# Kernel optimization log

Hardware: AMD Instinct MI355X
Metric: run time of the kernel (lower is better)

## Reference

```python
import jax, jax.numpy as jnp
import numpy as np

OBJ_DIM, REL_DIM, EFF_DIM = 5, 1, 100
REL_HID, OBJ_HID, OUT_DIM = 150, 100, 2


def _init_linear(key, fan_in, fan_out):
    kw, kb = jax.random.split(key)
    bound = 1.0 / np.sqrt(fan_in)
    W = jax.random.uniform(kw, (fan_in, fan_out), jnp.float32, -bound, bound)
    b = jax.random.uniform(kb, (fan_out,), jnp.float32, -bound, bound)
    return W, b


def setup_inputs() -> dict:
    key = jax.random.key(0)
    ks = jax.random.split(key, 12)
    B, N, R = 64, 100, 9900
    inp = {
        "objects": jax.random.normal(ks[0], (B, N, OBJ_DIM), jnp.float32),
        "sender_relations": jax.random.uniform(ks[1], (B, N, R), jnp.float32),
        "receiver_relations": jax.random.uniform(ks[2], (B, N, R), jnp.float32),
        "relation_info": jax.random.normal(ks[3], (B, R, REL_DIM), jnp.float32),
    }
    # relational MLP: (2*obj + rel) -> 150 -> 150 -> effect_dim, ReLU after each
    rW1, rb1 = _init_linear(ks[4], 2 * OBJ_DIM + REL_DIM, REL_HID)
    rW2, rb2 = _init_linear(ks[5], REL_HID, REL_HID)
    rW3, rb3 = _init_linear(ks[6], REL_HID, EFF_DIM)
    # object MLP: (obj + effect) -> 100 -> 100 -> 2
    oW1, ob1 = _init_linear(ks[7], OBJ_DIM + EFF_DIM, OBJ_HID)
    oW2, ob2 = _init_linear(ks[8], OBJ_HID, OBJ_HID)
    oW3, ob3 = _init_linear(ks[9], OBJ_HID, OUT_DIM)
    inp.update(rW1=rW1, rb1=rb1, rW2=rW2, rb2=rb2, rW3=rW3, rb3=rb3,
               oW1=oW1, ob1=ob1, oW2=oW2, ob2=ob2, oW3=oW3, ob3=ob3)
    return inp


def _relational_mlp(x, rW1, rb1, rW2, rb2, rW3, rb3):
    h = jax.nn.relu(x @ rW1 + rb1)
    h = jax.nn.relu(h @ rW2 + rb2)
    return jax.nn.relu(h @ rW3 + rb3)


def _object_mlp(x, oW1, ob1, oW2, ob2, oW3, ob3):
    h = jax.nn.relu(x @ oW1 + ob1)
    h = jax.nn.relu(h @ oW2 + ob2)
    return h @ oW3 + ob3


def reference(objects, sender_relations, receiver_relations, relation_info,
              rW1, rb1, rW2, rb2, rW3, rb3, oW1, ob1, oW2, ob2, oW3, ob3):
    # gather: [B,R,N] @ [B,N,D] -> [B,R,D]
    senders = jnp.einsum('bnr,bnd->brd', sender_relations, objects)
    receivers = jnp.einsum('bnr,bnd->brd', receiver_relations, objects)
    rel_in = jnp.concatenate([senders, receivers, relation_info], axis=2)
    effects = _relational_mlp(rel_in, rW1, rb1, rW2, rb2, rW3, rb3)  # [B,R,E]
    # scatter: [B,N,R] @ [B,R,E] -> [B,N,E]
    effect_receivers = jnp.einsum('bnr,bre->bne', receiver_relations, effects)
    obj_in = jnp.concatenate([objects, effect_receivers], axis=2)
    return _object_mlp(obj_in, oW1, ob1, oW2, ob2, oW3, ob3)  # [B,N,2]
```

## Files before the change

kernel.cpp:

```cpp
#include <hip/hip_runtime.h>
#include <hip/hip_bf16.h>

#define B_    64
#define N_    100
#define R_    9900
#define OBJD  5
#define EFF   100

typedef __bf16 bf16x8 __attribute__((ext_vector_type(8)));
typedef __bf16 bf16x2 __attribute__((ext_vector_type(2)));
typedef float  f32x4  __attribute__((ext_vector_type(4)));

__device__ __forceinline__ ushort f2bf(float f) {
    __bf16 h = (__bf16)f;
    return __builtin_bit_cast(ushort, h);
}
__device__ __forceinline__ unsigned pk2(float a, float b) {
    bf16x2 v; v[0] = (__bf16)a; v[1] = (__bf16)b;
    return __builtin_bit_cast(unsigned, v);
}
__device__ __forceinline__ float bf2f(ushort u) {
    union { unsigned u; float f; } x; x.u = ((unsigned)u) << 16;
    return x.f;
}

#define WTR_OBJ 52096
#define W2F_OFF 144256
#define W3F_OFF 169856

__global__ __launch_bounds__(256) void k_prepw(
    const float* __restrict__ W1, const float* __restrict__ W2,
    const float* __restrict__ W3, const float* __restrict__ O1,
    const float* __restrict__ O2, const float* __restrict__ O3,
    ushort* __restrict__ WTR)
{
    const int img = blockIdx.x;
    if (img == 0) {
        for (int idx = threadIdx.x; idx < 6400; idx += 256) {
            const int c = idx / 40, k = idx - (idx/40)*40;
            WTR[idx] = f2bf((c < 150 && k < 11) ? W1[k*150 + c] : 0.f);
        }
    } else if (img == 1) {
        for (int idx = threadIdx.x; idx < 26880; idx += 256) {
            const int c = idx / 168, k = idx - (idx/168)*168;
            WTR[6400 + idx] = f2bf((c < 150 && k < 150) ? W2[k*150 + c] : 0.f);
        }
    } else if (img == 2) {
        for (int idx = threadIdx.x; idx < 18816; idx += 256) {
            const int c = idx / 168, k = idx - (idx/168)*168;
            WTR[33280 + idx] = f2bf((c < 100 && k < 150) ? W3[k*100 + c] : 0.f);
        }
    } else if (img == 11) {
        for (int idx = threadIdx.x; idx < 25600; idx += 256) {
            const int ctks = idx >> 9;
            const int ct = ctks / 5, ks = ctks - ct*5;
            const int lane = (idx >> 3) & 63, e = idx & 7;
            const int c = ct*16 + (lane & 15);
            const int k = ks*32 + (lane >> 4)*8 + e;
            WTR[W2F_OFF + idx] = f2bf((c < 150 && k < 150) ? W2[k*150 + c] : 0.f);
        }
    } else if (img == 12) {
        for (int idx = threadIdx.x; idx < 17920; idx += 256) {
            const int ctks = idx >> 9;
            const int ct = ctks / 5, ks = ctks - ct*5;
            const int lane = (idx >> 3) & 63, e = idx & 7;
            const int c = ct*16 + (lane & 15);
            const int k = ks*32 + (lane >> 4)*8 + e;
            WTR[W3F_OFF + idx] = f2bf((c < 100 && k < 150) ? W3[k*100 + c] : 0.f);
        }
    } else {
        const int j = img - 3;
        ushort* dst = WTR + WTR_OBJ + (size_t)j*11520;
        for (int idx = threadIdx.x; idx < 11520; idx += 256) {
            const int cc = idx / 72, kk = idx - (idx/72)*72;
            float v = 0.f;
            if (kk < 64) {
                if (j < 4) {
                    const int kg = j*64 + kk;
                    int row = -1;
                    if (kg < 5) row = kg;
                    else if (kg >= 8 && kg < 108) row = kg - 3;
                    else if (kg >= 108 && kg < 208) row = kg - 103;
                    if (cc < 100 && row >= 0) v = O1[row*100 + cc];
                } else if (j < 6) {
                    const int kg = (j-4)*64 + kk;
                    if (cc < 100 && kg < 100) v = O2[kg*100 + cc];
                } else {
                    const int kg = (j-6)*64 + kk;
                    if (cc < 2 && kg < 100) v = O3[kg*2 + cc];
                }
            }
            dst[idx] = f2bf(v);
        }
    }
}

#define LW1   0
#define LBA   6400
#define LBB   14464
#define LACT  22528
#define LBIAS 33280
#define LGB   34080
#define LTOT  35616

__global__ __launch_bounds__(512, 2) void k_relmlp_p(
    const float* __restrict__ obj, const float* __restrict__ SR,
    const float* __restrict__ RR, const float* __restrict__ RI,
    const ushort* __restrict__ WTR,
    const float* __restrict__ b1, const float* __restrict__ b2,
    const float* __restrict__ b3, float* __restrict__ ER)
{
    __shared__ __align__(16) ushort lds[LTOT];
    const int t   = threadIdx.x;
    const int b   = blockIdx.x >> 3;
    const int oct = blockIdx.x & 7;
    const int lane = t & 63, w = t >> 6;
    const int lo = lane & 15, hi = lane >> 4;
    const int mt = w & 3, nh = w >> 2;
    const int q  = t & 7,  rr = t >> 3;

    ushort* bufA = lds + LBA;
    ushort* bufB = lds + LBB;
    ushort* act  = lds + LACT;
    ushort* gb   = lds + LGB;
    const float* bias = (const float*)(lds + LBIAS);

    #pragma unroll
    for (int j = 0; j < 2; ++j) {
        const int idx = t + j*512;
        if (idx < 800)
            reinterpret_cast<uint4*>(lds)[idx] =
                reinterpret_cast<const uint4*>(WTR)[idx];
    }
    {
        float* bias_w = (float*)(lds + LBIAS);
        if (t < 150)      bias_w[t] = b1[t];
        else if (t < 300) bias_w[t] = b2[t-150];
        else if (t < 400) bias_w[t] = b3[t-300];
    }
    if (t < 216) {
        ushort* base = ((t < 108) ? bufA : bufB) + 100*72;
        const int k = (t < 108) ? t : t - 108;
        *reinterpret_cast<uint4*>(base + k*8) = make_uint4(0u, 0u, 0u, 0u);
    }
    if (t < 64) {
        ushort* gb0 = gb + t*24;
        gb0[11] = 0;
        *reinterpret_cast<ushort4*>(&gb0[12]) = make_ushort4(0,0,0,0);
        *reinterpret_cast<ushort4*>(&gb0[16]) = make_ushort4(0,0,0,0);
        *reinterpret_cast<ushort4*>(&gb0[20]) = make_ushort4(0,0,0,0);
    }

    float objv[13][5];
    {
        const int n0 = q*13;
        #pragma unroll
        for (int i = 0; i < 13; ++i) {
            const int n = n0 + i;
            #pragma unroll
            for (int d = 0; d < 5; ++d)
                objv[i][d] = (n < N_) ? obj[(size_t)b*500 + n*5 + d] : 0.f;
        }
    }

    const int tile0 = (oct*155) >> 3;
    const int tile1 = ((oct+1)*155) >> 3;

    f32x4 acc_er[7];
    #pragma unroll
    for (int ct = 0; ct < 7; ++ct) acc_er[ct] = (f32x4){0.f, 0.f, 0.f, 0.f};

    float4 psr[4], prr[4];
    float pri = 0.f, pri_n = 0.f;
    auto load4 = [&](float4* p, const float* M, int tile) {
        const int rr0 = tile*64;
        const int nr = (R_ - rr0 < 64) ? R_ - rr0 : 64;
        #pragma unroll
        for (int i = 0; i < 4; ++i) {
            const int idx = t + i*512;
            const int ci = idx < 1600 ? idx : 1599;
            const int n = ci >> 4, qq = ci & 15;
            const int col = (qq*4 < nr) ? qq*4 : 0;
            p[i] = *reinterpret_cast<const float4*>(
                &M[((size_t)b*N_ + n)*R_ + rr0 + col]);
        }
    };
    auto store4 = [&](const float4* p, ushort* dst, int nrow) {
        #pragma unroll
        for (int i = 0; i < 4; ++i) {
            const int idx = t + i*512;
            if (idx < 1600) {
                const int n = idx >> 4, qq = idx & 15;
                float4 v = p[i];
                if (qq*4 >= nrow) v = make_float4(0.f, 0.f, 0.f, 0.f);
                uint2 u; u.x = pk2(v.x, v.y); u.y = pk2(v.z, v.w);
                *reinterpret_cast<uint2*>(&dst[n*72 + qq*4]) = u;
            }
        }
    };
    auto loadRI = [&](int tile) -> float {
        const int rr0 = tile*64;
        return (t < 64 && rr0 + t < R_) ? RI[(size_t)b*R_ + rr0 + t] : 0.f;
    };

    load4(psr, SR, tile0);
    load4(prr, RR, tile0);
    pri = loadRI(tile0);
    __syncthreads();

    for (int tile = tile0; tile < tile1; ++tile) {
        const int r0 = tile*64;
        const int nrow = (R_ - r0 < 64) ? R_ - r0 : 64;

        store4(psr, bufA, nrow);
        store4(prr, bufB, nrow);
        if (tile + 1 < tile1) {
            load4(psr, SR, tile+1);
            load4(prr, RR, tile+1);
            pri_n = loadRI(tile+1);
        }
        __syncthreads();

        {
            float s0=0.f,s1=0.f,s2=0.f,s3=0.f,s4=0.f;
            float g0=0.f,g1=0.f,g2=0.f,g3=0.f,g4=0.f;
            const int n0 = q*13;
            #pragma unroll
            for (int i = 0; i < 13; ++i) {
                const int n = n0 + i;
                const float ms = bf2f(bufA[n*72 + rr]);
                const float mr = bf2f(bufB[n*72 + rr]);
                s0 += ms*objv[i][0]; s1 += ms*objv[i][1]; s2 += ms*objv[i][2];
                s3 += ms*objv[i][3]; s4 += ms*objv[i][4];
                g0 += mr*objv[i][0]; g1 += mr*objv[i][1]; g2 += mr*objv[i][2];
                g3 += mr*objv[i][3]; g4 += mr*objv[i][4];
            }
            #pragma unroll
            for (int msk = 1; msk < 8; msk <<= 1) {
                s0 += __shfl_xor(s0, msk); s1 += __shfl_xor(s1, msk);
                s2 += __shfl_xor(s2, msk); s3 += __shfl_xor(s3, msk);
                s4 += __shfl_xor(s4, msk);
                g0 += __shfl_xor(g0, msk); g1 += __shfl_xor(g1, msk);
                g2 += __shfl_xor(g2, msk); g3 += __shfl_xor(g3, msk);
                g4 += __shfl_xor(g4, msk);
            }
            if (q < 5) {
                const float sv = (q==0)?s0:(q==1)?s1:(q==2)?s2:(q==3)?s3:s4;
                const float gv = (q==0)?g0:(q==1)?g1:(q==2)?g2:(q==3)?g3:g4;
                gb[rr*24 + q]     = f2bf(sv);
                gb[rr*24 + 5 + q] = f2bf(gv);
            }
            if (t < 64) gb[t*24 + 10] = f2bf(pri);
            pri = pri_n;
        }
        __syncthreads();

        {
            f32x4 acc[5];
            #pragma unroll
            for (int j = 0; j < 5; ++j) {
                const int c = (nh*5 + j)*16 + lo;
                const float bv = (c < 150) ? bias[c] : 0.f;
                acc[j][0]=bv; acc[j][1]=bv; acc[j][2]=bv; acc[j][3]=bv;
            }
            bf16x8 a = {};
            if (hi < 2)
                a = *reinterpret_cast<const bf16x8*>(
                    &gb[(mt*16 + lo)*24 + hi*8]);
            #pragma unroll
            for (int j = 0; j < 5; ++j) {
                const int ct = nh*5 + j;
                const bf16x8 bb = *reinterpret_cast<const bf16x8*>(
                    &lds[LW1 + (ct*16 + lo)*40 + hi*8]);
                acc[j] = __builtin_amdgcn_mfma_f32_16x16x32_bf16(a, bb, acc[j], 0,0,0);
            }
            #pragma unroll
            for (int j = 0; j < 5; ++j) {
                const int ct = nh*5 + j;
                #pragma unroll
                for (int r = 0; r < 4; ++r)
                    act[(mt*16 + hi*4 + r)*168 + ct*16 + lo] =
                        f2bf(fmaxf(acc[j][r], 0.f));
            }
            __syncthreads();
        }
        {
            const ushort* w2p = WTR + W2F_OFF + (size_t)lane*8 + (size_t)nh*12800;
            asm volatile("" : "+v"(w2p));
            f32x4 acc[5];
            #pragma unroll
            for (int j = 0; j < 5; ++j) {
                const int c = (nh*5 + j)*16 + lo;
                const float bv = (c < 150) ? bias[150 + c] : 0.f;
                acc[j][0]=bv; acc[j][1]=bv; acc[j][2]=bv; acc[j][3]=bv;
            }
            #pragma unroll
            for (int ks = 0; ks < 5; ++ks) {
                const bf16x8 a = *reinterpret_cast<const bf16x8*>(
                    &act[(mt*16 + lo)*168 + ks*32 + hi*8]);
                const bf16x8 b0  = *reinterpret_cast<const bf16x8*>(w2p + ((0*5 + ks) << 9));
                const bf16x8 b1v = *reinterpret_cast<const bf16x8*>(w2p + ((1*5 + ks) << 9));
                const bf16x8 b2v = *reinterpret_cast<const bf16x8*>(w2p + ((2*5 + ks) << 9));
                const bf16x8 b3v = *reinterpret_cast<const bf16x8*>(w2p + ((3*5 + ks) << 9));
                const bf16x8 b4v = *reinterpret_cast<const bf16x8*>(w2p + ((4*5 + ks) << 9));
                acc[0] = __builtin_amdgcn_mfma_f32_16x16x32_bf16(a, b0,  acc[0], 0,0,0);
                acc[1] = __builtin_amdgcn_mfma_f32_16x16x32_bf16(a, b1v, acc[1], 0,0,0);
                acc[2] = __builtin_amdgcn_mfma_f32_16x16x32_bf16(a, b2v, acc[2], 0,0,0);
                acc[3] = __builtin_amdgcn_mfma_f32_16x16x32_bf16(a, b3v, acc[3], 0,0,0);
                acc[4] = __builtin_amdgcn_mfma_f32_16x16x32_bf16(a, b4v, acc[4], 0,0,0);
            }
            __syncthreads();
            #pragma unroll
            for (int j = 0; j < 5; ++j) {
                const int ct = nh*5 + j;
                #pragma unroll
                for (int r = 0; r < 4; ++r)
                    act[(mt*16 + hi*4 + r)*168 + ct*16 + lo] =
                        f2bf(fmaxf(acc[j][r], 0.f));
            }
            __syncthreads();
        }
        {
            const ushort* w3p = WTR + W3F_OFF + (size_t)lane*8 + (size_t)nh*10240;
            asm volatile("" : "+v"(w3p));
            const int nct = nh ? 3 : 4;
            f32x4 acc[4];
            #pragma unroll
            for (int j = 0; j < 4; ++j) {
                const int c = (nh*4 + j)*16 + lo;
                const float bv = (c < 100) ? bias[300 + c] : 0.f;
                acc[j][0]=bv; acc[j][1]=bv; acc[j][2]=bv; acc[j][3]=bv;
            }
            #pragma unroll
            for (int ks = 0; ks < 5; ++ks) {
                const bf16x8 a = *reinterpret_cast<const bf16x8*>(
                    &act[(mt*16 + lo)*168 + ks*32 + hi*8]);
                #pragma unroll
                for (int j = 0; j < 4; ++j) {
                    if (j < nct) {
                        const bf16x8 bb = *reinterpret_cast<const bf16x8*>(
                            w3p + ((j*5 + ks) << 9));
                        acc[j] = __builtin_amdgcn_mfma_f32_16x16x32_bf16(a, bb, acc[j], 0,0,0);
                    }
                }
            }
            #pragma unroll
            for (int j = 0; j < 4; ++j) {
                if (j < nct) {
                    const int e = (nh*4 + j)*16 + lo;
                    if (e < 100) {
                        uint2 u;
                        u.x = pk2(fmaxf(acc[j][0], 0.f), fmaxf(acc[j][1], 0.f));
                        u.y = pk2(fmaxf(acc[j][2], 0.f), fmaxf(acc[j][3], 0.f));
                        *reinterpret_cast<uint2*>(&bufA[e*72 + mt*16 + hi*4]) = u;
                    }
                }
            }
            __syncthreads();
        }

        if (w < 7) {
            #pragma unroll
            for (int ks = 0; ks < 2; ++ks) {
                const bf16x8 a = *reinterpret_cast<const bf16x8*>(
                    &bufB[(w*16 + lo)*72 + ks*32 + hi*8]);
                #pragma unroll
                for (int ct = 0; ct < 7; ++ct) {
                    const bf16x8 bb = *reinterpret_cast<const bf16x8*>(
                        &bufA[(ct*16 + lo)*72 + ks*32 + hi*8]);
                    acc_er[ct] = __builtin_amdgcn_mfma_f32_16x16x32_bf16(
                        a, bb, acc_er[ct], 0, 0, 0);
                }
            }
        }
        __syncthreads();
    }

    if (w < 7) {
        float* ERq = ER + ((size_t)oct*B_ + b)*(size_t)(N_*EFF);
        #pragma unroll
        for (int ct = 0; ct < 7; ++ct) {
            const int e = ct*16 + lo;
            if (e < EFF) {
                #pragma unroll
                for (int rg = 0; rg < 4; ++rg) {
                    const int n = w*16 + hi*4 + rg;
                    if (n < N_)
                        ERq[n*EFF + e] = acc_er[ct][rg];
                }
            }
        }
    }
}

__device__ __forceinline__ void img_load(const ushort* __restrict__ g,
                                         uint4* pre, int t) {
    #pragma unroll
    for (int j = 0; j < 6; ++j) {
        int idx = t + j*256;
        int cidx = idx < 1440 ? idx : 1439;
        pre[j] = *reinterpret_cast<const uint4*>(g + (size_t)cidx*8);
    }
}
__device__ __forceinline__ void img_store(const uint4* pre, ushort* wt, int t) {
    #pragma unroll
    for (int j = 0; j < 6; ++j) {
        int idx = t + j*256;
        if (idx < 1440)
            *reinterpret_cast<uint4*>(wt + (size_t)idx*8) = pre[j];
    }
}

template<int COUT, int NCHUNK, int LASTKS, int NCT, bool RELU, int EPI, int ASTR>
__device__ __forceinline__ void mfma_layerO(
    const ushort* __restrict__ WT, const float* __restrict__ Bias,
    ushort* act, ushort* wt, int t, float* gout, int grow0)
{
    const int lane = t & 63;
    const int wv   = t >> 6;
    const int lo   = lane & 15;
    const int hi   = lane >> 4;

    f32x4 acc[2][NCT];
    #pragma unroll
    for (int ct = 0; ct < NCT; ++ct) {
        const int c = ct*16 + lo;
        const float bv = (c < COUT) ? Bias[c] : 0.f;
        #pragma unroll
        for (int m = 0; m < 2; ++m) {
            acc[m][ct][0] = bv; acc[m][ct][1] = bv;
            acc[m][ct][2] = bv; acc[m][ct][3] = bv;
        }
    }

    uint4 pre[6];
    img_load(WT, pre, t);
    #pragma unroll
    for (int q = 0; q < NCHUNK; ++q) {
        __syncthreads();
        img_store(pre, wt, t);
        if (q + 1 < NCHUNK) img_load(WT + (size_t)(q+1)*11520, pre, t);
        __syncthreads();
        const int nks = (q == NCHUNK-1) ? LASTKS : 2;
        #pragma unroll
        for (int ks = 0; ks < 2; ++ks) {
            if (ks < nks) {
                const int kg = q*64 + ks*32;
                const bf16x8 a0 = *reinterpret_cast<const bf16x8*>(
                    &act[(wv*32 +      lo)*ASTR + kg + hi*8]);
                const bf16x8 a1 = *reinterpret_cast<const bf16x8*>(
                    &act[(wv*32 + 16 + lo)*ASTR + kg + hi*8]);
                #pragma unroll
                for (int ct = 0; ct < NCT; ++ct) {
                    const bf16x8 b = *reinterpret_cast<const bf16x8*>(
                        &wt[(ct*16 + lo)*72 + ks*32 + hi*8]);
                    acc[0][ct] = __builtin_amdgcn_mfma_f32_16x16x32_bf16(
                        a0, b, acc[0][ct], 0, 0, 0);
                    acc[1][ct] = __builtin_amdgcn_mfma_f32_16x16x32_bf16(
                        a1, b, acc[1][ct], 0, 0, 0);
                }
            }
        }
    }

    __syncthreads();
    if (EPI == 0) {
        #pragma unroll
        for (int m = 0; m < 2; ++m)
            #pragma unroll
            for (int ct = 0; ct < NCT; ++ct)
                #pragma unroll
                for (int r = 0; r < 4; ++r) {
                    float v = acc[m][ct][r];
                    if (RELU) v = fmaxf(v, 0.f);
                    act[(wv*32 + m*16 + hi*4 + r)*ASTR + ct*16 + lo] = f2bf(v);
                }
    } else {
        #pragma unroll
        for (int m = 0; m < 2; ++m)
            #pragma unroll
            for (int r = 0; r < 4; ++r)
                if (lo < 2)
                    gout[(size_t)(grow0 + wv*32 + m*16 + hi*4 + r)*2 + lo] =
                        acc[m][0][r];
    }
    __syncthreads();
}

#define OSTR 232
#define ERSL ((size_t)B_*N_*EFF)

__global__ __launch_bounds__(256, 1) void k_objmlp_mfma(
    const float* __restrict__ obj, const float* __restrict__ ER,
    const ushort* __restrict__ WO,
    const float* __restrict__ ob1, const float* __restrict__ ob2,
    const float* __restrict__ ob3, float* __restrict__ out)
{
    __shared__ __align__(16) ushort act[128*OSTR];
    __shared__ __align__(16) ushort wt[160*72];
    const int t = threadIdx.x;
    const int rowbase = blockIdx.x * 128;

    float4 per[13];
    #pragma unroll
    for (int j = 0; j < 13; ++j) {
        const int idx = t + j*256;
        const int ci = idx < 3200 ? idx : 3199;
        const int row = ci / 25, c = ci - row*25;
        const float* p = &ER[(size_t)(rowbase + row)*100 + c*4];
        float4 s = make_float4(0.f, 0.f, 0.f, 0.f);
        #pragma unroll
        for (int sl = 0; sl < 8; ++sl) {
            const float4 a = *reinterpret_cast<const float4*>(p + (size_t)sl*ERSL);
            s.x += a.x; s.y += a.y; s.z += a.z; s.w += a.w;
        }
        per[j] = s;
    }
    #pragma unroll
    for (int j = 0; j < 13; ++j) {
        const int idx = t + j*256;
        if (idx < 3200) {
            const int row = idx / 25, c = idx - row*25;
            ushort h[4], l[4];
            #pragma unroll
            for (int k = 0; k < 4; ++k) {
                const float f = ((const float*)&per[j])[k];
                h[k] = f2bf(f);
                l[k] = f2bf(f - bf2f(h[k]));
            }
            *reinterpret_cast<ushort4*>(&act[row*OSTR + 8 + c*4]) =
                make_ushort4(h[0], h[1], h[2], h[3]);
            *reinterpret_cast<ushort4*>(&act[row*OSTR + 108 + c*4]) =
                make_ushort4(l[0], l[1], l[2], l[3]);
        }
    }
    #pragma unroll
    for (int j = 0; j < 3; ++j) {
        const int idx = t + j*256;
        if (idx < 640) {
            const int row = idx / 5, d = idx - row*5;
            act[row*OSTR + d] = f2bf(obj[(size_t)(rowbase + row)*5 + d]);
        }
    }
    #pragma unroll
    for (int j = 0; j < 2; ++j) {
        const int idx = t + j*256;
        if (idx < 384) {
            const int row = idx / 3, c = 5 + (idx - row*3);
            act[row*OSTR + c] = 0;
        }
    }
    #pragma unroll
    for (int j = 0; j < 2; ++j) {
        const int idx = t + j*256;
        if (idx < 512) {
            const int row = idx >> 2, p = idx & 3;
            *reinterpret_cast<ushort4*>(&act[row*OSTR + 208 + p*4]) =
                make_ushort4(0, 0, 0, 0);
        }
    }

    mfma_layerO<100, 4, 1, 7, true,  0, OSTR>(WO,           ob1, act, wt, t, nullptr, 0);
    mfma_layerO<100, 2, 2, 7, true,  0, OSTR>(WO + 4*11520, ob2, act, wt, t, nullptr, 0);
    mfma_layerO<2,   2, 2, 1, false, 2, OSTR>(WO + 6*11520, ob3, act, wt, t, out, rowbase);
}

extern "C" void kernel_launch(void* const* d_in, const int* in_sizes, int n_in,
                              void* d_out, int out_size, void* d_ws, size_t ws_size,
                              hipStream_t stream)
{
    const float* objects = (const float*)d_in[0];
    const float* SR      = (const float*)d_in[1];
    const float* RR      = (const float*)d_in[2];
    const float* RI      = (const float*)d_in[3];
    const float* rW1 = (const float*)d_in[4];  const float* rb1 = (const float*)d_in[5];
    const float* rW2 = (const float*)d_in[6];  const float* rb2 = (const float*)d_in[7];
    const float* rW3 = (const float*)d_in[8];  const float* rb3 = (const float*)d_in[9];
    const float* oW1 = (const float*)d_in[10]; const float* ob1 = (const float*)d_in[11];
    const float* oW2 = (const float*)d_in[12]; const float* ob2 = (const float*)d_in[13];
    const float* oW3 = (const float*)d_in[14]; const float* ob3 = (const float*)d_in[15];
    float* out = (float*)d_out;

    char* ws = (char*)d_ws;
    float*  ERp = (float*)ws;
    ushort* WTR = (ushort*)(ws + (size_t)8*B_*N_*EFF*sizeof(float));

    k_prepw<<<dim3(13), 256, 0, stream>>>(rW1, rW2, rW3, oW1, oW2, oW3, WTR);

    k_relmlp_p<<<dim3(512), 512, 0, stream>>>(objects, SR, RR, RI, WTR,
                                              rb1, rb2, rb3, ERp);

    k_objmlp_mfma<<<dim3(50), 256, 0, stream>>>(objects, ERp, WTR + WTR_OBJ,
                                                ob1, ob2, ob3, out);
}
```

Before: 399.5 us.

## Compute sender/receiver gather with MFMA via transposed LDS tiles

Replaces the scalar per-thread gather (objv register array, dot products, shuffle reductions) with MFMA matmuls. SR and RR tiles are stored transposed in LDS and multiplied against bf16 objects held in LDS. W1 fragments are prepacked in MFMA layout and read from global memory instead of LDS. The cost is an extra global load per element of RR (both a transposed copy and the original layout), strided scalar global loads for the transposed tiles, and a larger LDS footprint, all meant to cut VALU and shuffle work.

```diff
diff --git a/kernel.cpp b/kernel.cpp
--- a/kernel.cpp
+++ b/kernel.cpp
@@ -27,6 +27,7 @@
 #define WTR_OBJ 52096
 #define W2F_OFF 144256
 #define W3F_OFF 169856
+#define W1F_OFF 187776
 
 __global__ __launch_bounds__(256) void k_prepw(
     const float* __restrict__ W1, const float* __restrict__ W2,
@@ -67,6 +68,14 @@
             const int c = ct*16 + (lane & 15);
             const int k = ks*32 + (lane >> 4)*8 + e;
             WTR[W3F_OFF + idx] = f2bf((c < 100 && k < 150) ? W3[k*100 + c] : 0.f);
+        }
+    } else if (img == 13) {
+        for (int idx = threadIdx.x; idx < 5120; idx += 256) {
+            const int ct = idx >> 9;
+            const int lane = (idx >> 3) & 63, e = idx & 7;
+            const int c = ct*16 + (lane & 15);
+            const int k = (lane >> 4)*8 + e;
+            WTR[W1F_OFF + idx] = f2bf((c < 150 && k < 11) ? W1[k*150 + c] : 0.f);
         }
     } else {
         const int j = img - 3;
@@ -95,13 +104,15 @@
     }
 }
 
-#define LW1   0
-#define LBA   6400
-#define LBB   14464
-#define LACT  22528
-#define LBIAS 33280
-#define LGB   34080
-#define LTOT  35616
+#define STRT  136
+#define LSRT  0
+#define LRRT  8704
+#define LBB   17408
+#define LACT  25472
+#define LBIAS 36224
+#define LGB   37024
+#define LOBJ  38560
+#define LTOT  40736
 
 __global__ __launch_bounds__(512, 2) void k_relmlp_p(
     const float* __restrict__ obj, const float* __restrict__ SR,
@@ -117,20 +128,29 @@
     const int lane = t & 63, w = t >> 6;
     const int lo = lane & 15, hi = lane >> 4;
     const int mt = w & 3, nh = w >> 2;
-    const int q  = t & 7,  rr = t >> 3;
-
-    ushort* bufA = lds + LBA;
-    ushort* bufB = lds + LBB;
+
+    ushort* SRT  = lds + LSRT;
+    ushort* RRT  = lds + LRRT;
+    ushort* RRn  = lds + LBB;
+    ushort* EB   = lds + LSRT;
     ushort* act  = lds + LACT;
     ushort* gb   = lds + LGB;
+    ushort* lobj = lds + LOBJ;
     const float* bias = (const float*)(lds + LBIAS);
 
     #pragma unroll
-    for (int j = 0; j < 2; ++j) {
+    for (int j = 0; j < 5; ++j) {
         const int idx = t + j*512;
-        if (idx < 800)
-            reinterpret_cast<uint4*>(lds)[idx] =
-                reinterpret_cast<const uint4*>(WTR)[idx];
+        if (idx < 2176)
+            reinterpret_cast<uint4*>(lds)[idx] = make_uint4(0u,0u,0u,0u);
+    }
+    #pragma unroll
+    for (int j = 0; j < 5; ++j) {
+        const int idx = t + j*512;
+        if (idx < 2176) {
+            const int d = idx / STRT, n = idx - d*STRT;
+            lobj[idx] = f2bf((d < 5 && n < N_) ? obj[(size_t)b*500 + n*5 + d] : 0.f);
+        }
     }
     {
         float* bias_w = (float*)(lds + LBIAS);
@@ -138,10 +158,8 @@
         else if (t < 300) bias_w[t] = b2[t-150];
         else if (t < 400) bias_w[t] = b3[t-300];
     }
-    if (t < 216) {
-        ushort* base = ((t < 108) ? bufA : bufB) + 100*72;
-        const int k = (t < 108) ? t : t - 108;
-        *reinterpret_cast<uint4*>(base + k*8) = make_uint4(0u, 0u, 0u, 0u);
+    if (t < 108) {
+        *reinterpret_cast<uint4*>(RRn + 100*72 + t*8) = make_uint4(0u,0u,0u,0u);
     }
     if (t < 64) {
         ushort* gb0 = gb + t*24;
@@ -151,27 +169,33 @@
         *reinterpret_cast<ushort4*>(&gb0[20]) = make_ushort4(0,0,0,0);
     }
 
-    float objv[13][5];
-    {
-        const int n0 = q*13;
+    const int tile0 = (oct*155) >> 3;
+    const int tile1 = ((oct+1)*155) >> 3;
+
+    f32x4 acc_er[7];
+    #pragma unroll
+    for (int ct = 0; ct < 7; ++ct) acc_er[ct] = (f32x4){0.f, 0.f, 0.f, 0.f};
+
+    float vs[13], vr[13];
+    auto loadT = [&](float* v, const float* M, int tile) {
+        const int rr0 = tile*64;
+        const int r = t & 63, g = t >> 6;
+        const int n0 = g*13;
+        const bool rok = (rr0 + r < R_);
         #pragma unroll
         for (int i = 0; i < 13; ++i) {
             const int n = n0 + i;
-            #pragma unroll
-            for (int d = 0; d < 5; ++d)
-                objv[i][d] = (n < N_) ? obj[(size_t)b*500 + n*5 + d] : 0.f;
-        }
-    }
-
-    const int tile0 = (oct*155) >> 3;
-    const int tile1 = ((oct+1)*155) >> 3;
-
-    f32x4 acc_er[7];
-    #pragma unroll
-    for (int ct = 0; ct < 7; ++ct) acc_er[ct] = (f32x4){0.f, 0.f, 0.f, 0.f};
-
-    float4 psr[4], prr[4];
-    float pri = 0.f, pri_n = 0.f;
+            v[i] = (rok && n < N_) ? M[((size_t)b*N_ + n)*R_ + rr0 + r] : 0.f;
+        }
+    };
+    auto storeT = [&](const float* v, ushort* dst) {
+        const int r = t & 63, g = t >> 6;
+        const int n0 = g*13;
+        #pragma unroll
+        for (int i = 0; i < 13; ++i)
+            dst[r*STRT + n0 + i] = f2bf(v[i]);
+    };
+    float4 prr[4];
     auto load4 = [&](float4* p, const float* M, int tile) {
         const int rr0 = tile*64;
         const int nr = (R_ - rr0 < 64) ? R_ - rr0 : 64;
@@ -203,52 +227,43 @@
         return (t < 64 && rr0 + t < R_) ? RI[(size_t)b*R_ + rr0 + t] : 0.f;
     };
 
-    load4(psr, SR, tile0);
+    loadT(vs, SR, tile0);
+    loadT(vr, RR, tile0);
     load4(prr, RR, tile0);
-    pri = loadRI(tile0);
+    float pri = loadRI(tile0), pri_n = 0.f;
     __syncthreads();
 
     for (int tile = tile0; tile < tile1; ++tile) {
         const int r0 = tile*64;
         const int nrow = (R_ - r0 < 64) ? R_ - r0 : 64;
 
-        store4(psr, bufA, nrow);
-        store4(prr, bufB, nrow);
+        storeT(vs, SRT);
+        storeT(vr, RRT);
+        store4(prr, RRn, nrow);
         if (tile + 1 < tile1) {
-            load4(psr, SR, tile+1);
+            loadT(vs, SR, tile+1);
+            loadT(vr, RR, tile+1);
             load4(prr, RR, tile+1);
             pri_n = loadRI(tile+1);
         }
         __syncthreads();
 
         {
-            float s0=0.f,s1=0.f,s2=0.f,s3=0.f,s4=0.f;
-            float g0=0.f,g1=0.f,g2=0.f,g3=0.f,g4=0.f;
-            const int n0 = q*13;
-            #pragma unroll
-            for (int i = 0; i < 13; ++i) {
-                const int n = n0 + i;
-                const float ms = bf2f(bufA[n*72 + rr]);
-                const float mr = bf2f(bufB[n*72 + rr]);
-                s0 += ms*objv[i][0]; s1 += ms*objv[i][1]; s2 += ms*objv[i][2];
-                s3 += ms*objv[i][3]; s4 += ms*objv[i][4];
-                g0 += mr*objv[i][0]; g1 += mr*objv[i][1]; g2 += mr*objv[i][2];
-                g3 += mr*objv[i][3]; g4 += mr*objv[i][4];
-            }
-            #pragma unroll
-            for (int msk = 1; msk < 8; msk <<= 1) {
-                s0 += __shfl_xor(s0, msk); s1 += __shfl_xor(s1, msk);
-                s2 += __shfl_xor(s2, msk); s3 += __shfl_xor(s3, msk);
-                s4 += __shfl_xor(s4, msk);
-                g0 += __shfl_xor(g0, msk); g1 += __shfl_xor(g1, msk);
-                g2 += __shfl_xor(g2, msk); g3 += __shfl_xor(g3, msk);
-                g4 += __shfl_xor(g4, msk);
-            }
-            if (q < 5) {
-                const float sv = (q==0)?s0:(q==1)?s1:(q==2)?s2:(q==3)?s3:s4;
-                const float gv = (q==0)?g0:(q==1)?g1:(q==2)?g2:(q==3)?g3:g4;
-                gb[rr*24 + q]     = f2bf(sv);
-                gb[rr*24 + 5 + q] = f2bf(gv);
+            const int which = w >> 2;
+            const ushort* At = which ? RRT : SRT;
+            f32x4 g = (f32x4){0.f, 0.f, 0.f, 0.f};
+            #pragma unroll
+            for (int ks = 0; ks < 4; ++ks) {
+                const bf16x8 a = *reinterpret_cast<const bf16x8*>(
+                    &At[(mt*16 + lo)*STRT + ks*32 + hi*8]);
+                const bf16x8 bO = *reinterpret_cast<const bf16x8*>(
+                    &lobj[lo*STRT + ks*32 + hi*8]);
+                g = __builtin_amdgcn_mfma_f32_16x16x32_bf16(a, bO, g, 0,0,0);
+            }
+            if (lo < 5) {
+                #pragma unroll
+                for (int r = 0; r < 4; ++r)
+                    gb[(mt*16 + hi*4 + r)*24 + which*5 + lo] = f2bf(g[r]);
             }
             if (t < 64) gb[t*24 + 10] = f2bf(pri);
             pri = pri_n;
@@ -256,6 +271,8 @@
         __syncthreads();
 
         {
+            const ushort* w1p = WTR + W1F_OFF + (size_t)lane*8;
+            asm volatile("" : "+v"(w1p));
             f32x4 acc[5];
             #pragma unroll
             for (int j = 0; j < 5; ++j) {
@@ -270,8 +287,7 @@
             #pragma unroll
             for (int j = 0; j < 5; ++j) {
                 const int ct = nh*5 + j;
-                const bf16x8 bb = *reinterpret_cast<const bf16x8*>(
-                    &lds[LW1 + (ct*16 + lo)*40 + hi*8]);
+                const bf16x8 bb = *reinterpret_cast<const bf16x8*>(w1p + ct*512);
                 acc[j] = __builtin_amdgcn_mfma_f32_16x16x32_bf16(a, bb, acc[j], 0,0,0);
             }
             #pragma unroll
@@ -348,12 +364,12 @@
             for (int j = 0; j < 4; ++j) {
                 if (j < nct) {
                     const int e = (nh*4 + j)*16 + lo;
+                    uint2 u = make_uint2(0u, 0u);
                     if (e < 100) {
-                        uint2 u;
                         u.x = pk2(fmaxf(acc[j][0], 0.f), fmaxf(acc[j][1], 0.f));
                         u.y = pk2(fmaxf(acc[j][2], 0.f), fmaxf(acc[j][3], 0.f));
-                        *reinterpret_cast<uint2*>(&bufA[e*72 + mt*16 + hi*4]) = u;
                     }
+                    *reinterpret_cast<uint2*>(&EB[e*72 + mt*16 + hi*4]) = u;
                 }
             }
             __syncthreads();
@@ -363,11 +379,11 @@
             #pragma unroll
             for (int ks = 0; ks < 2; ++ks) {
                 const bf16x8 a = *reinterpret_cast<const bf16x8*>(
-                    &bufB[(w*16 + lo)*72 + ks*32 + hi*8]);
+                    &RRn[(w*16 + lo)*72 + ks*32 + hi*8]);
                 #pragma unroll
                 for (int ct = 0; ct < 7; ++ct) {
                     const bf16x8 bb = *reinterpret_cast<const bf16x8*>(
-                        &bufA[(ct*16 + lo)*72 + ks*32 + hi*8]);
+                        &EB[(ct*16 + lo)*72 + ks*32 + hi*8]);
                     acc_er[ct] = __builtin_amdgcn_mfma_f32_16x16x32_bf16(
                         a, bb, acc_er[ct], 0, 0, 0);
                 }
@@ -585,7 +601,7 @@
     float*  ERp = (float*)ws;
     ushort* WTR = (ushort*)(ws + (size_t)8*B_*N_*EFF*sizeof(float));
 
-    k_prepw<<<dim3(13), 256, 0, stream>>>(rW1, rW2, rW3, oW1, oW2, oW3, WTR);
+    k_prepw<<<dim3(14), 256, 0, stream>>>(rW1, rW2, rW3, oW1, oW2, oW3, WTR);
 
     k_relmlp_p<<<dim3(512), 512, 0, stream>>>(objects, SR, RR, RI, WTR,
                                               rb1, rb2, rb3, ERp);
```

Result: slower. 429.6 us (+7.5%).

## Warp-specialize relational MLP kernel into compute and load/scatter warp groups

Applied to the files above, without the earlier changes.

Splits the 8 waves of the relational-MLP block into two roles. Waves 0-3 run the gather and the three MLP layers on 16-row slices each, with per-wave activation buffers. Waves 4-7 stage the next tile of sender/receiver matrices into double-buffered LDS and perform the scatter MFMA for the previous tile, leaving one barrier per tile. This is meant to overlap global loads and the scatter with MLP compute and remove several barriers. In exchange LDS use roughly doubles and launch bounds drop to one block per CU, which lowers occupancy.

```diff
diff --git a/kernel.cpp b/kernel.cpp
--- a/kernel.cpp
+++ b/kernel.cpp
@@ -96,14 +96,19 @@
 }
 
 #define LW1   0
-#define LBA   6400
-#define LBB   14464
-#define LACT  22528
-#define LBIAS 33280
-#define LGB   34080
-#define LTOT  35616
-
-__global__ __launch_bounds__(512, 2) void k_relmlp_p(
+#define LSR0  6400
+#define LSR1  14464
+#define LRR0  22528
+#define LRR1  30592
+#define LEB0  38656
+#define LEB1  46720
+#define LACT1 54784
+#define LACT2 65536
+#define LGB   76288
+#define LBIAS 77824
+#define LTOT  78624
+
+__global__ __launch_bounds__(512, 1) void k_relmlp_p(
     const float* __restrict__ obj, const float* __restrict__ SR,
     const float* __restrict__ RR, const float* __restrict__ RI,
     const ushort* __restrict__ WTR,
@@ -116,14 +121,10 @@
     const int oct = blockIdx.x & 7;
     const int lane = t & 63, w = t >> 6;
     const int lo = lane & 15, hi = lane >> 4;
-    const int mt = w & 3, nh = w >> 2;
-    const int q  = t & 7,  rr = t >> 3;
-
-    ushort* bufA = lds + LBA;
-    ushort* bufB = lds + LBB;
-    ushort* act  = lds + LACT;
-    ushort* gb   = lds + LGB;
+
     const float* bias = (const float*)(lds + LBIAS);
+    const int tile0 = (oct*155) >> 3;
+    const int tile1 = ((oct+1)*155) >> 3;
 
     #pragma unroll
     for (int j = 0; j < 2; ++j) {
@@ -138,255 +139,278 @@
         else if (t < 300) bias_w[t] = b2[t-150];
         else if (t < 400) bias_w[t] = b3[t-300];
     }
-    if (t < 216) {
-        ushort* base = ((t < 108) ? bufA : bufB) + 100*72;
-        const int k = (t < 108) ? t : t - 108;
-        *reinterpret_cast<uint4*>(base + k*8) = make_uint4(0u, 0u, 0u, 0u);
+    #pragma unroll
+    for (int j = 0; j < 2; ++j) {
+        const int idx = t + j*512;
+        if (idx < 648) {
+            const int bsel = idx / 108, kk = idx - bsel*108;
+            *reinterpret_cast<uint4*>(lds + LSR0 + bsel*8064 + 100*72 + kk*8) =
+                make_uint4(0u, 0u, 0u, 0u);
+        }
     }
     if (t < 64) {
-        ushort* gb0 = gb + t*24;
+        ushort* gb0 = lds + LGB + (t >> 4)*384 + (t & 15)*24;
         gb0[11] = 0;
         *reinterpret_cast<ushort4*>(&gb0[12]) = make_ushort4(0,0,0,0);
         *reinterpret_cast<ushort4*>(&gb0[16]) = make_ushort4(0,0,0,0);
         *reinterpret_cast<ushort4*>(&gb0[20]) = make_ushort4(0,0,0,0);
     }
 
-    float objv[13][5];
-    {
-        const int n0 = q*13;
-        #pragma unroll
-        for (int i = 0; i < 13; ++i) {
-            const int n = n0 + i;
-            #pragma unroll
-            for (int d = 0; d < 5; ++d)
-                objv[i][d] = (n < N_) ? obj[(size_t)b*500 + n*5 + d] : 0.f;
-        }
-    }
-
-    const int tile0 = (oct*155) >> 3;
-    const int tile1 = ((oct+1)*155) >> 3;
-
-    f32x4 acc_er[7];
-    #pragma unroll
-    for (int ct = 0; ct < 7; ++ct) acc_er[ct] = (f32x4){0.f, 0.f, 0.f, 0.f};
-
-    float4 psr[4], prr[4];
-    float pri = 0.f, pri_n = 0.f;
-    auto load4 = [&](float4* p, const float* M, int tile) {
+    const int tS = t - 256;
+    auto stage = [&](int tile, int pp) {
         const int rr0 = tile*64;
         const int nr = (R_ - rr0 < 64) ? R_ - rr0 : 64;
-        #pragma unroll
-        for (int i = 0; i < 4; ++i) {
-            const int idx = t + i*512;
-            const int ci = idx < 1600 ? idx : 1599;
-            const int n = ci >> 4, qq = ci & 15;
-            const int col = (qq*4 < nr) ? qq*4 : 0;
-            p[i] = *reinterpret_cast<const float4*>(
-                &M[((size_t)b*N_ + n)*R_ + rr0 + col]);
-        }
-    };
-    auto store4 = [&](const float4* p, ushort* dst, int nrow) {
-        #pragma unroll
-        for (int i = 0; i < 4; ++i) {
-            const int idx = t + i*512;
+        ushort* dS = lds + (pp ? LSR1 : LSR0);
+        ushort* dR = lds + (pp ? LRR1 : LRR0);
+        #pragma unroll
+        for (int i = 0; i < 7; ++i) {
+            const int idx = tS + i*256;
             if (idx < 1600) {
                 const int n = idx >> 4, qq = idx & 15;
-                float4 v = p[i];
-                if (qq*4 >= nrow) v = make_float4(0.f, 0.f, 0.f, 0.f);
+                const int col = (qq*4 < nr) ? qq*4 : 0;
+                float4 v = *reinterpret_cast<const float4*>(
+                    &SR[((size_t)b*N_ + n)*R_ + rr0 + col]);
+                if (qq*4 >= nr) v = make_float4(0.f, 0.f, 0.f, 0.f);
                 uint2 u; u.x = pk2(v.x, v.y); u.y = pk2(v.z, v.w);
-                *reinterpret_cast<uint2*>(&dst[n*72 + qq*4]) = u;
+                *reinterpret_cast<uint2*>(&dS[n*72 + qq*4]) = u;
+                float4 v2 = *reinterpret_cast<const float4*>(
+                    &RR[((size_t)b*N_ + n)*R_ + rr0 + col]);
+                if (qq*4 >= nr) v2 = make_float4(0.f, 0.f, 0.f, 0.f);
+                uint2 u2; u2.x = pk2(v2.x, v2.y); u2.y = pk2(v2.z, v2.w);
+                *reinterpret_cast<uint2*>(&dR[n*72 + qq*4]) = u2;
             }
         }
     };
-    auto loadRI = [&](int tile) -> float {
-        const int rr0 = tile*64;
-        return (t < 64 && rr0 + t < R_) ? RI[(size_t)b*R_ + rr0 + t] : 0.f;
-    };
-
-    load4(psr, SR, tile0);
-    load4(prr, RR, tile0);
-    pri = loadRI(tile0);
+
+    if (w >= 4) stage(tile0, tile0 & 1);
     __syncthreads();
 
-    for (int tile = tile0; tile < tile1; ++tile) {
-        const int r0 = tile*64;
-        const int nrow = (R_ - r0 < 64) ? R_ - r0 : 64;
-
-        store4(psr, bufA, nrow);
-        store4(prr, bufB, nrow);
-        if (tile + 1 < tile1) {
-            load4(psr, SR, tile+1);
-            load4(prr, RR, tile+1);
-            pri_n = loadRI(tile+1);
-        }
-        __syncthreads();
-
+    if (w < 4) {
+        const int m = w;
+        ushort* act1m = lds + LACT1 + m*2688;
+        ushort* act2m = lds + LACT2 + m*2688;
+        ushort* gbm   = lds + LGB   + m*384;
+        const int q = lane & 7, rl = lane >> 3;
+
+        float objv[13][5];
         {
-            float s0=0.f,s1=0.f,s2=0.f,s3=0.f,s4=0.f;
-            float g0=0.f,g1=0.f,g2=0.f,g3=0.f,g4=0.f;
             const int n0 = q*13;
             #pragma unroll
             for (int i = 0; i < 13; ++i) {
                 const int n = n0 + i;
-                const float ms = bf2f(bufA[n*72 + rr]);
-                const float mr = bf2f(bufB[n*72 + rr]);
-                s0 += ms*objv[i][0]; s1 += ms*objv[i][1]; s2 += ms*objv[i][2];
-                s3 += ms*objv[i][3]; s4 += ms*objv[i][4];
-                g0 += mr*objv[i][0]; g1 += mr*objv[i][1]; g2 += mr*objv[i][2];
-                g3 += mr*objv[i][3]; g4 += mr*objv[i][4];
-            }
+                #pragma unroll
+                for (int d = 0; d < 5; ++d)
+                    objv[i][d] = (n < N_) ? obj[(size_t)b*500 + n*5 + d] : 0.f;
+            }
+        }
+
+        for (int k = tile0; k < tile1; ++k) {
+            const int p = k & 1;
+            const int r0 = k*64;
+            ushort* bufS = lds + (p ? LSR1 : LSR0);
+            ushort* bufR = lds + (p ? LRR1 : LRR0);
+            ushort* eb   = lds + (p ? LEB1 : LEB0);
+
             #pragma unroll
-            for (int msk = 1; msk < 8; msk <<= 1) {
-                s0 += __shfl_xor(s0, msk); s1 += __shfl_xor(s1, msk);
-                s2 += __shfl_xor(s2, msk); s3 += __shfl_xor(s3, msk);
-                s4 += __shfl_xor(s4, msk);
-                g0 += __shfl_xor(g0, msk); g1 += __shfl_xor(g1, msk);
-                g2 += __shfl_xor(g2, msk); g3 += __shfl_xor(g3, msk);
-                g4 += __shfl_xor(g4, msk);
-            }
-            if (q < 5) {
-                const float sv = (q==0)?s0:(q==1)?s1:(q==2)?s2:(q==3)?s3:s4;
-                const float gv = (q==0)?g0:(q==1)?g1:(q==2)?g2:(q==3)?g3:g4;
-                gb[rr*24 + q]     = f2bf(sv);
-                gb[rr*24 + 5 + q] = f2bf(gv);
-            }
-            if (t < 64) gb[t*24 + 10] = f2bf(pri);
-            pri = pri_n;
-        }
-        __syncthreads();
-
-        {
-            f32x4 acc[5];
+            for (int h = 0; h < 2; ++h) {
+                const int lr = h*8 + rl;
+                const int rT = m*16 + lr;
+                float s0=0.f,s1=0.f,s2=0.f,s3=0.f,s4=0.f;
+                float g0=0.f,g1=0.f,g2=0.f,g3=0.f,g4=0.f;
+                const int n0 = q*13;
+                #pragma unroll
+                for (int i = 0; i < 13; ++i) {
+                    const int n = n0 + i;
+                    const float ms = bf2f(bufS[n*72 + rT]);
+                    const float mr = bf2f(bufR[n*72 + rT]);
+                    s0 += ms*objv[i][0]; s1 += ms*objv[i][1]; s2 += ms*objv[i][2];
+                    s3 += ms*objv[i][3]; s4 += ms*objv[i][4];
+                    g0 += mr*objv[i][0]; g1 += mr*objv[i][1]; g2 += mr*objv[i][2];
+                    g3 += mr*objv[i][3]; g4 += mr*objv[i][4];
+                }
+                #pragma unroll
+                for (int msk = 1; msk < 8; msk <<= 1) {
+                    s0 += __shfl_xor(s0, msk); s1 += __shfl_xor(s1, msk);
+                    s2 += __shfl_xor(s2, msk); s3 += __shfl_xor(s3, msk);
+                    s4 += __shfl_xor(s4, msk);
+                    g0 += __shfl_xor(g0, msk); g1 += __shfl_xor(g1, msk);
+                    g2 += __shfl_xor(g2, msk); g3 += __shfl_xor(g3, msk);
+                    g4 += __shfl_xor(g4, msk);
+                }
+                if (q < 5) {
+                    const float sv = (q==0)?s0:(q==1)?s1:(q==2)?s2:(q==3)?s3:s4;
+                    const float gv = (q==0)?g0:(q==1)?g1:(q==2)?g2:(q==3)?g3:g4;
+                    gbm[lr*24 + q]     = f2bf(sv);
+                    gbm[lr*24 + 5 + q] = f2bf(gv);
+                } else if (q == 5) {
+                    const int rg = r0 + rT;
+                    gbm[lr*24 + 10] =
+                        f2bf((rg < R_) ? RI[(size_t)b*R_ + rg] : 0.f);
+                }
+            }
+
+            {
+                bf16x8 a = {};
+                if (hi < 2)
+                    a = *reinterpret_cast<const bf16x8*>(&gbm[lo*24 + hi*8]);
+                #pragma unroll
+                for (int half = 0; half < 2; ++half) {
+                    f32x4 acc[5];
+                    #pragma unroll
+                    for (int j = 0; j < 5; ++j) {
+                        const int c = (half*5 + j)*16 + lo;
+                        const float bv = (c < 150) ? bias[c] : 0.f;
+                        acc[j][0]=bv; acc[j][1]=bv; acc[j][2]=bv; acc[j][3]=bv;
+                    }
+                    #pragma unroll
+                    for (int j = 0; j < 5; ++j) {
+                        const int ct = half*5 + j;
+                        const bf16x8 bb = *reinterpret_cast<const bf16x8*>(
+                            &lds[LW1 + (ct*16 + lo)*40 + hi*8]);
+                        acc[j] = __builtin_amdgcn_mfma_f32_16x16x32_bf16(a, bb, acc[j], 0,0,0);
+                    }
+                    #pragma unroll
+                    for (int j = 0; j < 5; ++j)
+                        #pragma unroll
+                        for (int r = 0; r < 4; ++r)
+                            act1m[(hi*4 + r)*168 + (half*5 + j)*16 + lo] =
+                                f2bf(fmaxf(acc[j][r], 0.f));
+                }
+            }
+            {
+                const ushort* w2p = WTR + W2F_OFF + (size_t)lane*8;
+                asm volatile("" : "+v"(w2p));
+                #pragma unroll
+                for (int half = 0; half < 2; ++half) {
+                    f32x4 acc[5];
+                    #pragma unroll
+                    for (int j = 0; j < 5; ++j) {
+                        const int c = (half*5 + j)*16 + lo;
+                        const float bv = (c < 150) ? bias[150 + c] : 0.f;
+                        acc[j][0]=bv; acc[j][1]=bv; acc[j][2]=bv; acc[j][3]=bv;
+                    }
+                    #pragma unroll
+                    for (int ks = 0; ks < 5; ++ks) {
+                        const bf16x8 a = *reinterpret_cast<const bf16x8*>(
+                            &act1m[lo*168 + ks*32 + hi*8]);
+                        #pragma unroll
+                        for (int j = 0; j < 5; ++j) {
+                            const int ct = half*5 + j;
+                            const bf16x8 bb = *reinterpret_cast<const bf16x8*>(
+                                w2p + ((ct*5 + ks) << 9));
+                            acc[j] = __builtin_amdgcn_mfma_f32_16x16x32_bf16(
+                                a, bb, acc[j], 0,0,0);
+                        }
+                    }
+                    #pragma unroll
+                    for (int j = 0; j < 5; ++j)
+                        #pragma unroll
+                        for (int r = 0; r < 4; ++r)
+                            act2m[(hi*4 + r)*168 + (half*5 + j)*16 + lo] =
+                                f2bf(fmaxf(acc[j][r], 0.f));
+                }
+            }
+            {
+                const ushort* w3p = WTR + W3F_OFF + (size_t)lane*8;
+                asm volatile("" : "+v"(w3p));
+                #pragma unroll
+                for (int pass = 0; pass < 2; ++pass) {
+                    const int nct = pass ? 3 : 4;
+                    f32x4 acc[4];
+                    #pragma unroll
+                    for (int j = 0; j < 4; ++j) {
+                        const int c = (pass*4 + j)*16 + lo;
+                        const float bv = (j < nct && c < 100) ? bias[300 + c] : 0.f;
+                        acc[j][0]=bv; acc[j][1]=bv; acc[j][2]=bv; acc[j][3]=bv;
+                    }
+                    #pragma unroll
+                    for (int ks = 0; ks < 5; ++ks) {
+                        const bf16x8 a = *reinterpret_cast<const bf16x8*>(
+                            &act2m[lo*168 + ks*32 + hi*8]);
+                        #pragma unroll
+                        for (int j = 0; j < 4; ++j) {
+                            if (j < nct) {
+                                const int ct = pass*4 + j;
+                                const bf16x8 bb = *reinterpret_cast<const bf16x8*>(
+                                    w3p + ((ct*5 + ks) << 9));
+                                acc[j] = __builtin_amdgcn_mfma_f32_16x16x32_bf16(
+                                    a, bb, acc[j], 0,0,0);
+                            }
+                        }
+                    }
+                    #pragma unroll
+                    for (int j = 0; j < 4; ++j) {
+                        if (j < nct) {
+                            const int e = (pass*4 + j)*16 + lo;
+                            if (e < 100) {
+                                uint2 u;
+                                u.x = pk2(fmaxf(acc[j][0], 0.f), fmaxf(acc[j][1], 0.f));
+                                u.y = pk2(fmaxf(acc[j][2], 0.f), fmaxf(acc[j][3], 0.f));
+                                *reinterpret_cast<uint2*>(
+                                    &eb[e*72 + m*16 + hi*4]) = u;
+                            }
+                        }
+                    }
+                }
+            }
+            __syncthreads();
+        }
+    } else {
+        const int s = w - 4;
+        f32x4 acc_er[2][7];
+        #pragma unroll
+        for (int part = 0; part < 2; ++part)
             #pragma unroll
-            for (int j = 0; j < 5; ++j) {
-                const int c = (nh*5 + j)*16 + lo;
-                const float bv = (c < 150) ? bias[c] : 0.f;
-                acc[j][0]=bv; acc[j][1]=bv; acc[j][2]=bv; acc[j][3]=bv;
-            }
-            bf16x8 a = {};
-            if (hi < 2)
-                a = *reinterpret_cast<const bf16x8*>(
-                    &gb[(mt*16 + lo)*24 + hi*8]);
+            for (int ct = 0; ct < 7; ++ct)
+                acc_er[part][ct] = (f32x4){0.f, 0.f, 0.f, 0.f};
+
+        auto scat = [&](int pp) {
+            ushort* bufR = lds + (pp ? LRR1 : LRR0);
+            ushort* eb   = lds + (pp ? LEB1 : LEB0);
             #pragma unroll
-            for (int j = 0; j < 5; ++j) {
-                const int ct = nh*5 + j;
-                const bf16x8 bb = *reinterpret_cast<const bf16x8*>(
-                    &lds[LW1 + (ct*16 + lo)*40 + hi*8]);
-                acc[j] = __builtin_amdgcn_mfma_f32_16x16x32_bf16(a, bb, acc[j], 0,0,0);
-            }
-            #pragma unroll
-            for (int j = 0; j < 5; ++j) {
-                const int ct = nh*5 + j;
-                #pragma unroll
-                for (int r = 0; r < 4; ++r)
-                    act[(mt*16 + hi*4 + r)*168 + ct*16 + lo] =
-                        f2bf(fmaxf(acc[j][r], 0.f));
-            }
+            for (int part = 0; part < 2; ++part) {
+                const int nt = s + part*4;
+                if (nt < 7) {
+                    #pragma unroll
+                    for (int ks = 0; ks < 2; ++ks) {
+                        const bf16x8 a = *reinterpret_cast<const bf16x8*>(
+                            &bufR[(nt*16 + lo)*72 + ks*32 + hi*8]);
+                        #pragma unroll
+                        for (int ct = 0; ct < 7; ++ct) {
+                            const bf16x8 bb = *reinterpret_cast<const bf16x8*>(
+                                &eb[(ct*16 + lo)*72 + ks*32 + hi*8]);
+                            acc_er[part][ct] = __builtin_amdgcn_mfma_f32_16x16x32_bf16(
+                                a, bb, acc_er[part][ct], 0, 0, 0);
+                        }
+                    }
+                }
+            }
+        };
+
+        for (int k = tile0; k < tile1; ++k) {
+            const int p = k & 1;
+            if (k > tile0) scat(p ^ 1);
+            if (k + 1 < tile1) stage(k + 1, (k + 1) & 1);
             __syncthreads();
         }
-        {
-            const ushort* w2p = WTR + W2F_OFF + (size_t)lane*8 + (size_t)nh*12800;
-            asm volatile("" : "+v"(w2p));
-            f32x4 acc[5];
-            #pragma unroll
-            for (int j = 0; j < 5; ++j) {
-                const int c = (nh*5 + j)*16 + lo;
-                const float bv = (c < 150) ? bias[150 + c] : 0.f;
-                acc[j][0]=bv; acc[j][1]=bv; acc[j][2]=bv; acc[j][3]=bv;
-            }
-            #pragma unroll
-            for (int ks = 0; ks < 5; ++ks) {
-                const bf16x8 a = *reinterpret_cast<const bf16x8*>(
-                    &act[(mt*16 + lo)*168 + ks*32 + hi*8]);
-                const bf16x8 b0  = *reinterpret_cast<const bf16x8*>(w2p + ((0*5 + ks) << 9));
-                const bf16x8 b1v = *reinterpret_cast<const bf16x8*>(w2p + ((1*5 + ks) << 9));
-                const bf16x8 b2v = *reinterpret_cast<const bf16x8*>(w2p + ((2*5 + ks) << 9));
-                const bf16x8 b3v = *reinterpret_cast<const bf16x8*>(w2p + ((3*5 + ks) << 9));
-                const bf16x8 b4v = *reinterpret_cast<const bf16x8*>(w2p + ((4*5 + ks) << 9));
-                acc[0] = __builtin_amdgcn_mfma_f32_16x16x32_bf16(a, b0,  acc[0], 0,0,0);
-                acc[1] = __builtin_amdgcn_mfma_f32_16x16x32_bf16(a, b1v, acc[1], 0,0,0);
-                acc[2] = __builtin_amdgcn_mfma_f32_16x16x32_bf16(a, b2v, acc[2], 0,0,0);
-                acc[3] = __builtin_amdgcn_mfma_f32_16x16x32_bf16(a, b3v, acc[3], 0,0,0);
-                acc[4] = __builtin_amdgcn_mfma_f32_16x16x32_bf16(a, b4v, acc[4], 0,0,0);
-            }
-            __syncthreads();
-            #pragma unroll
-            for (int j = 0; j < 5; ++j) {
-                const int ct = nh*5 + j;
-                #pragma unroll
-                for (int r = 0; r < 4; ++r)
-                    act[(mt*16 + hi*4 + r)*168 + ct*16 + lo] =
-                        f2bf(fmaxf(acc[j][r], 0.f));
-            }
-            __syncthreads();
-        }
-        {
-            const ushort* w3p = WTR + W3F_OFF + (size_t)lane*8 + (size_t)nh*10240;
-            asm volatile("" : "+v"(w3p));
-            const int nct = nh ? 3 : 4;
-            f32x4 acc[4];
-            #pragma unroll
-            for (int j = 0; j < 4; ++j) {
-                const int c = (nh*4 + j)*16 + lo;
-                const float bv = (c < 100) ? bias[300 + c] : 0.f;
-                acc[j][0]=bv; acc[j][1]=bv; acc[j][2]=bv; acc[j][3]=bv;
-            }
-            #pragma unroll
-            for (int ks = 0; ks < 5; ++ks) {
-                const bf16x8 a = *reinterpret_cast<const bf16x8*>(
-                    &act[(mt*16 + lo)*168 + ks*32 + hi*8]);
-                #pragma unroll
-                for (int j = 0; j < 4; ++j) {
-                    if (j < nct) {
-                        const bf16x8 bb = *reinterpret_cast<const bf16x8*>(
-                            w3p + ((j*5 + ks) << 9));
-                        acc[j] = __builtin_amdgcn_mfma_f32_16x16x32_bf16(a, bb, acc[j], 0,0,0);
-                    }
-                }
-            }
-            #pragma unroll
-            for (int j = 0; j < 4; ++j) {
-                if (j < nct) {
-                    const int e = (nh*4 + j)*16 + lo;
-                    if (e < 100) {
-                        uint2 u;
-                        u.x = pk2(fmaxf(acc[j][0], 0.f), fmaxf(acc[j][1], 0.f));
-                        u.y = pk2(fmaxf(acc[j][2], 0.f), fmaxf(acc[j][3], 0.f));
-                        *reinterpret_cast<uint2*>(&bufA[e*72 + mt*16 + hi*4]) = u;
-                    }
-                }
-            }
-            __syncthreads();
-        }
-
-        if (w < 7) {
-            #pragma unroll
-            for (int ks = 0; ks < 2; ++ks) {
-                const bf16x8 a = *reinterpret_cast<const bf16x8*>(
-                    &bufB[(w*16 + lo)*72 + ks*32 + hi*8]);
+        scat((tile1 - 1) & 1);
+
+        float* ERq = ER + ((size_t)oct*B_ + b)*(size_t)(N_*EFF);
+        #pragma unroll
+        for (int part = 0; part < 2; ++part) {
+            const int nt = s + part*4;
+            if (nt < 7) {
                 #pragma unroll
                 for (int ct = 0; ct < 7; ++ct) {
-                    const bf16x8 bb = *reinterpret_cast<const bf16x8*>(
-                        &bufA[(ct*16 + lo)*72 + ks*32 + hi*8]);
-                    acc_er[ct] = __builtin_amdgcn_mfma_f32_16x16x32_bf16(
-                        a, bb, acc_er[ct], 0, 0, 0);
-                }
-            }
-        }
-        __syncthreads();
-    }
-
-    if (w < 7) {
-        float* ERq = ER + ((size_t)oct*B_ + b)*(size_t)(N_*EFF);
-        #pragma unroll
-        for (int ct = 0; ct < 7; ++ct) {
-            const int e = ct*16 + lo;
-            if (e < EFF) {
-                #pragma unroll
-                for (int rg = 0; rg < 4; ++rg) {
-                    const int n = w*16 + hi*4 + rg;
-                    if (n < N_)
-                        ERq[n*EFF + e] = acc_er[ct][rg];
+                    const int e = ct*16 + lo;
+                    if (e < EFF) {
+                        #pragma unroll
+                        for (int rg = 0; rg < 4; ++rg) {
+                            const int n = nt*16 + hi*4 + rg;
+                            if (n < N_)
+                                ERq[n*EFF + e] = acc_er[part][ct][rg];
+                        }
+                    }
                 }
             }
         }
```

New measurement: 441.0 us. 10.4% more time.
